# Performance work log

Measured on AMD Instinct MI355X. Metric: run time of the kernel, lower is better.

## Reference

```python
import jax, jax.numpy as jnp
import numpy as np

B, T, F, U, H = 256, 512, 128, 256, 64


def setup_inputs() -> dict:
    key = jax.random.key(0)
    k0, k1, k2, k3, k4 = jax.random.split(key, 5)
    x = jax.random.normal(k0, (B, T, F), dtype=jnp.float32)
    # Keras RandomUniform default range (-0.05, 0.05) for LSTM kernel/bias
    kernel = jax.random.uniform(k1, (F, 4 * U), minval=-0.05, maxval=0.05, dtype=jnp.float32)
    rec_kernel = jax.random.uniform(k2, (U, 4 * U), minval=-0.05, maxval=0.05, dtype=jnp.float32)
    bias = jax.random.uniform(k3, (4 * U,), minval=-0.05, maxval=0.05, dtype=jnp.float32)
    # Dense head: glorot-ish scale for the big [T*U, H] weight
    w_out = jax.random.normal(k4, (T * U, H), dtype=jnp.float32) * (1.0 / np.sqrt(T * U))
    b_out = jnp.zeros((H,), dtype=jnp.float32)
    return {"x": x, "kernel": kernel, "rec_kernel": rec_kernel, "bias": bias,
            "w_out": w_out, "b_out": b_out}


def _lstm_swish(x, kernel, rec_kernel, bias):
    """Keras LSTM with activation=swish, recurrent_activation=sigmoid.
    Gate order along last axis: i, f, c(g), o. Returns full hidden sequence [B,T,U]."""
    b, t, _ = x.shape
    u = rec_kernel.shape[0]
    # Precompute input projections for all timesteps: [B,T,4U]
    xz = jnp.einsum('btf,fg->btg', x, kernel) + bias

    def step(carry, xz_t):
        h, c = carry
        z = xz_t + h @ rec_kernel  # [B,4U]
        zi, zf, zg, zo = jnp.split(z, 4, axis=-1)
        i = jax.nn.sigmoid(zi)
        f = jax.nn.sigmoid(zf)
        g = jax.nn.swish(zg)
        o = jax.nn.sigmoid(zo)
        c_new = f * c + i * g
        h_new = o * jax.nn.swish(c_new)
        return (h_new, c_new), h_new

    h0 = jnp.zeros((b, u), dtype=x.dtype)
    c0 = jnp.zeros((b, u), dtype=x.dtype)
    (_, _), hs = jax.lax.scan(step, (h0, c0), jnp.swapaxes(xz, 0, 1))  # hs: [T,B,U]
    return jnp.swapaxes(hs, 0, 1)  # [B,T,U]


def reference(x, kernel, rec_kernel, bias, w_out, b_out):
    seq = _lstm_swish(x, kernel, rec_kernel, bias)        # [B,T,U]
    flat = seq.reshape(seq.shape[0], -1)                   # [B,T*U]
    return flat @ w_out + b_out                            # [B,horizon]
```

## Files before the change

kernel.cpp:

```cpp
#include <hip/hip_runtime.h>
#include <stdint.h>

#define B_ 256
#define T_ 512
#define F_ 128
#define U_ 256
#define H_ 64
#define G4U (4 * U_)

typedef __attribute__((ext_vector_type(8))) short short8;
typedef __attribute__((ext_vector_type(4))) float f32x4;
typedef unsigned long long ull;

__device__ __forceinline__ uint16_t f2bf(float f) {
  uint32_t u = __builtin_bit_cast(uint32_t, f);
  u += 0x7fffu + ((u >> 16) & 1u);
  return (uint16_t)(u >> 16);
}
__device__ __forceinline__ float sigm(float z) {
  return 1.0f / (1.0f + __expf(-z));
}

__global__ __launch_bounds__(256, 1) void lstm_kernel(
    const float* __restrict__ x, const float* __restrict__ kern,
    const float* __restrict__ rker, const float* __restrict__ bias,
    uint16_t* __restrict__ seq, uint16_t* __restrict__ hbuf,
    uint32_t* __restrict__ ctr)
{
  const int tid  = threadIdx.x;
  const int lane = tid & 63;
  const int wv   = tid >> 6;
  const int bg   = blockIdx.x & 15;
  const int ug   = blockIdx.x >> 4;

  __shared__ __align__(16) uint16_t x_stage[4][64][8];
  __shared__ __align__(16) uint16_t h_stage[8][64][8];
  __shared__ __align__(16) float    z_stage[128][20];

  short8 wf[2][8];
  short8 kf[2][4];
  float  bias_r[2];
  #pragma unroll
  for (int i2 = 0; i2 < 2; ++i2) {
    const int ct   = wv * 2 + i2;
    const int cloc = ct * 16 + (lane & 15);
    const int gcol = (cloc >> 5) * U_ + ug * 32 + (cloc & 31);
    bias_r[i2] = bias[gcol];
    #pragma unroll
    for (int kt = 0; kt < 8; ++kt) {
      short8 v;
      #pragma unroll
      for (int j = 0; j < 8; ++j) {
        const int k = kt * 32 + (lane >> 4) * 8 + j;
        v[j] = (short)f2bf(rker[(size_t)k * G4U + gcol]);
      }
      wf[i2][kt] = v;
    }
    #pragma unroll
    for (int kt = 0; kt < 4; ++kt) {
      short8 v;
      #pragma unroll
      for (int j = 0; j < 8; ++j) {
        const int k = kt * 32 + (lane >> 4) * 8 + j;
        v[j] = (short)f2bf(kern[(size_t)k * G4U + gcol]);
      }
      kf[i2][kt] = v;
    }
  }

  const int xrow = tid & 15;
  const int xfb  = (tid >> 6) * 32 + ((tid >> 4) & 3) * 8;
  const int hrow0 = (tid * 2) & 15;
  const int hub0  = (tid >> 5) * 32 + ((tid >> 3) & 3) * 8;
  const int gr  = tid & 15;
  const int u0  = (tid >> 4) * 2;

  float cst0 = 0.f, cst1 = 0.f;

  float xp[8];
  {
    const float* p = x + ((size_t)(bg * 16 + xrow) * T_ + 0) * F_ + xfb;
    #pragma unroll
    for (int j = 0; j < 8; ++j) xp[j] = p[j];
    uint16_t* d = (uint16_t*)x_stage + tid * 8;
    #pragma unroll
    for (int j = 0; j < 8; ++j) d[j] = f2bf(xp[j]);
  }
  __syncthreads();

  for (int t = 0; t < T_; ++t) {
    f32x4 acc0 = {bias_r[0], bias_r[0], bias_r[0], bias_r[0]};
    f32x4 acc1 = {bias_r[1], bias_r[1], bias_r[1], bias_r[1]};
    #pragma unroll
    for (int kt = 0; kt < 4; ++kt) {
      short8 a = *(const short8*)&x_stage[kt][lane][0];
      acc0 = __builtin_amdgcn_mfma_f32_16x16x32_bf16(a, kf[0][kt], acc0, 0, 0, 0);
      acc1 = __builtin_amdgcn_mfma_f32_16x16x32_bf16(a, kf[1][kt], acc1, 0, 0, 0);
    }
    {
      const int tn = (t + 1 < T_) ? t + 1 : t;
      const float* p = x + ((size_t)(bg * 16 + xrow) * T_ + tn) * F_ + xfb;
      #pragma unroll
      for (int j = 0; j < 8; ++j) xp[j] = p[j];
    }
    {
      const uint32_t target = 8u * (uint32_t)t;
      while (__hip_atomic_load(&ctr[bg], __ATOMIC_RELAXED, __HIP_MEMORY_SCOPE_AGENT) < target)
        __builtin_amdgcn_s_sleep(2);
      __builtin_amdgcn_sched_barrier(0);
    }
    {
      const int cur = t & 1;
      const ull* p = (const ull*)(hbuf + (size_t)cur * (B_ * U_)
                                  + (size_t)(bg * 16 + hrow0) * U_ + hub0);
      ull a0 = __hip_atomic_load(p,      __ATOMIC_RELAXED, __HIP_MEMORY_SCOPE_AGENT);
      ull a1 = __hip_atomic_load(p + 1,  __ATOMIC_RELAXED, __HIP_MEMORY_SCOPE_AGENT);
      ull a2 = __hip_atomic_load(p + 64, __ATOMIC_RELAXED, __HIP_MEMORY_SCOPE_AGENT);
      ull a3 = __hip_atomic_load(p + 65, __ATOMIC_RELAXED, __HIP_MEMORY_SCOPE_AGENT);
      ull* d = (ull*)h_stage + (size_t)tid * 4;
      d[0] = a0; d[1] = a1; d[2] = a2; d[3] = a3;
    }
    __syncthreads();
    #pragma unroll
    for (int kt = 0; kt < 8; ++kt) {
      short8 a = *(const short8*)&h_stage[kt][lane][0];
      acc0 = __builtin_amdgcn_mfma_f32_16x16x32_bf16(a, wf[0][kt], acc0, 0, 0, 0);
      acc1 = __builtin_amdgcn_mfma_f32_16x16x32_bf16(a, wf[1][kt], acc1, 0, 0, 0);
    }
    {
      const int c0 = (wv * 2 + 0) * 16 + (lane & 15);
      const int c1 = (wv * 2 + 1) * 16 + (lane & 15);
      const int r0 = (lane >> 4) * 4;
      *(f32x4*)&z_stage[c0][r0] = acc0;
      *(f32x4*)&z_stage[c1][r0] = acc1;
    }
    __syncthreads();
    {
      const float zi0 = z_stage[u0][gr],      zi1 = z_stage[u0 + 1][gr];
      const float zf0 = z_stage[32 + u0][gr], zf1 = z_stage[33 + u0][gr];
      const float zg0 = z_stage[64 + u0][gr], zg1 = z_stage[65 + u0][gr];
      const float zo0 = z_stage[96 + u0][gr], zo1 = z_stage[97 + u0][gr];
      const float i0 = sigm(zi0), i1 = sigm(zi1);
      const float f0 = sigm(zf0), f1 = sigm(zf1);
      const float g0 = zg0 * sigm(zg0), g1 = zg1 * sigm(zg1);
      const float o0 = sigm(zo0), o1 = sigm(zo1);
      cst0 = f0 * cst0 + i0 * g0;
      cst1 = f1 * cst1 + i1 * g1;
      const float h0 = o0 * (cst0 * sigm(cst0));
      const float h1 = o1 * (cst1 * sigm(cst1));
      const uint32_t packed = (uint32_t)f2bf(h0) | ((uint32_t)f2bf(h1) << 16);
      const int nxt = (t + 1) & 1;
      uint32_t* hd = (uint32_t*)(hbuf + (size_t)nxt * (B_ * U_)
                                 + (size_t)(bg * 16 + gr) * U_ + ug * 32 + u0);
      __hip_atomic_store(hd, packed, __ATOMIC_RELAXED, __HIP_MEMORY_SCOPE_AGENT);
      *(uint32_t*)(seq + ((size_t)(bg * 16 + gr) * T_ + t) * U_ + ug * 32 + u0) = packed;
      uint16_t* d = (uint16_t*)x_stage + tid * 8;
      #pragma unroll
      for (int j = 0; j < 8; ++j) d[j] = f2bf(xp[j]);
    }
    __syncthreads();
    if (tid == 0)
      (void)__hip_atomic_fetch_add(&ctr[bg], 1u, __ATOMIC_RELAXED, __HIP_MEMORY_SCOPE_AGENT);
  }
}

__global__ __launch_bounds__(256, 1) void head_kernel(
    const uint16_t* __restrict__ seq, const float* __restrict__ w_out,
    float* __restrict__ partials)
{
  const int g    = blockIdx.x;
  const int tid  = threadIdx.x;
  const int lane = tid & 63;
  const int wv   = tid >> 6;

  f32x4 acc[4][4];
  #pragma unroll
  for (int i = 0; i < 4; ++i)
    #pragma unroll
    for (int c = 0; c < 4; ++c) acc[i][c] = (f32x4){0.f, 0.f, 0.f, 0.f};

  for (int ks = 0; ks < 64; ++ks) {
    const int krow = g * 2048 + ks * 32 + (lane >> 4) * 8;
    short8 bf[4];
    #pragma unroll
    for (int c = 0; c < 4; ++c) {
      short8 v;
      #pragma unroll
      for (int j = 0; j < 8; ++j)
        v[j] = (short)f2bf(w_out[(size_t)(krow + j) * H_ + c * 16 + (lane & 15)]);
      bf[c] = v;
    }
    #pragma unroll
    for (int i = 0; i < 4; ++i) {
      const int b = (wv * 4 + i) * 16 + (lane & 15);
      short8 a = *(const short8*)(seq + (size_t)b * (T_ * U_) + krow);
      #pragma unroll
      for (int c = 0; c < 4; ++c)
        acc[i][c] = __builtin_amdgcn_mfma_f32_16x16x32_bf16(a, bf[c], acc[i][c], 0, 0, 0);
    }
  }
  #pragma unroll
  for (int i = 0; i < 4; ++i)
    #pragma unroll
    for (int c = 0; c < 4; ++c)
      #pragma unroll
      for (int r = 0; r < 4; ++r) {
        const int b = wv * 64 + i * 16 + (lane >> 4) * 4 + r;
        partials[((size_t)g * B_ + b) * H_ + c * 16 + (lane & 15)] = acc[i][c][r];
      }
}

__global__ void reduce_kernel(const float* __restrict__ partials,
                              const float* __restrict__ b_out,
                              float* __restrict__ out)
{
  const int i = blockIdx.x * 256 + threadIdx.x;
  float s = b_out[i & (H_ - 1)];
  #pragma unroll 8
  for (int g = 0; g < 64; ++g) s += partials[(size_t)g * (B_ * H_) + i];
  out[i] = s;
}

extern "C" void kernel_launch(void* const* d_in, const int* in_sizes, int n_in,
                              void* d_out, int out_size, void* d_ws, size_t ws_size,
                              hipStream_t stream) {
  (void)in_sizes; (void)n_in; (void)out_size; (void)ws_size;
  const float* x     = (const float*)d_in[0];
  const float* kern  = (const float*)d_in[1];
  const float* rker  = (const float*)d_in[2];
  const float* bias  = (const float*)d_in[3];
  const float* w_out = (const float*)d_in[4];
  const float* b_out = (const float*)d_in[5];
  float* out = (float*)d_out;

  char* ws = (char*)d_ws;
  const size_t seq_bytes  = (size_t)B_ * T_ * U_ * 2;
  const size_t hbuf_bytes = (size_t)2 * B_ * U_ * 2;
  uint16_t* seq      = (uint16_t*)ws;
  uint16_t* hbuf     = (uint16_t*)(ws + seq_bytes);
  uint32_t* ctr      = (uint32_t*)(ws + seq_bytes + hbuf_bytes);
  float*    partials = (float*)(ws + seq_bytes + hbuf_bytes + 256);

  hipMemsetAsync(hbuf, 0, (size_t)B_ * U_ * 2, stream);
  hipMemsetAsync(ctr, 0, 64, stream);

  lstm_kernel<<<128, 256, 0, stream>>>(x, kern, rker, bias, seq, hbuf, ctr);
  head_kernel<<<64, 256, 0, stream>>>(seq, w_out, partials);
  reduce_kernel<<<64, 256, 0, stream>>>(partials, b_out, out);
}
```

Before: 1.447 ms.

## Replace counter-based inter-block sync with sequence-tagged hidden-state words

Every hidden-state value is now written as a 64-bit word whose upper half holds the timestep tag. Consumers spin directly on the data until all tags match, so the per-group atomic counter, its increment and the trailing block barrier go away. The x staging write moves before the gate barrier, the first step skips the recurrent matmul, and __syncthreads is replaced by a raw waitcnt plus s_barrier. This removes one barrier and one global atomic round trip from the serial critical path. In exchange it doubles the bytes of h traffic and relies on the atomic 64-bit stores and loads being seen whole.

```diff
diff --git a/kernel.cpp b/kernel.cpp
--- a/kernel.cpp
+++ b/kernel.cpp
@@ -10,7 +10,10 @@
 
 typedef __attribute__((ext_vector_type(8))) short short8;
 typedef __attribute__((ext_vector_type(4))) float f32x4;
+typedef __attribute__((ext_vector_type(4))) uint32_t u32x4;
 typedef unsigned long long ull;
+
+#define BARRIER_LDS() asm volatile("s_waitcnt lgkmcnt(0)\ns_barrier" ::: "memory")
 
 __device__ __forceinline__ uint16_t f2bf(float f) {
   uint32_t u = __builtin_bit_cast(uint32_t, f);
@@ -20,12 +23,14 @@
 __device__ __forceinline__ float sigm(float z) {
   return 1.0f / (1.0f + __expf(-z));
 }
+__device__ __forceinline__ ull ald(const ull* p) {
+  return __hip_atomic_load(p, __ATOMIC_RELAXED, __HIP_MEMORY_SCOPE_AGENT);
+}
 
 __global__ __launch_bounds__(256, 1) void lstm_kernel(
     const float* __restrict__ x, const float* __restrict__ kern,
     const float* __restrict__ rker, const float* __restrict__ bias,
-    uint16_t* __restrict__ seq, uint16_t* __restrict__ hbuf,
-    uint32_t* __restrict__ ctr)
+    uint16_t* __restrict__ seq, ull* __restrict__ hbuf)
 {
   const int tid  = threadIdx.x;
   const int lane = tid & 63;
@@ -70,10 +75,10 @@
 
   const int xrow = tid & 15;
   const int xfb  = (tid >> 6) * 32 + ((tid >> 4) & 3) * 8;
-  const int hrow0 = (tid * 2) & 15;
-  const int hub0  = (tid >> 5) * 32 + ((tid >> 3) & 3) * 8;
   const int gr  = tid & 15;
   const int u0  = (tid >> 4) * 2;
+  const int erow = lane & 15;
+  const int ec0  = (tid >> 6) * 16 + ((lane >> 4) & 3) * 4;
 
   float cst0 = 0.f, cst1 = 0.f;
 
@@ -103,29 +108,34 @@
       #pragma unroll
       for (int j = 0; j < 8; ++j) xp[j] = p[j];
     }
-    {
-      const uint32_t target = 8u * (uint32_t)t;
-      while (__hip_atomic_load(&ctr[bg], __ATOMIC_RELAXED, __HIP_MEMORY_SCOPE_AGENT) < target)
-        __builtin_amdgcn_s_sleep(2);
-      __builtin_amdgcn_sched_barrier(0);
-    }
-    {
-      const int cur = t & 1;
-      const ull* p = (const ull*)(hbuf + (size_t)cur * (B_ * U_)
-                                  + (size_t)(bg * 16 + hrow0) * U_ + hub0);
-      ull a0 = __hip_atomic_load(p,      __ATOMIC_RELAXED, __HIP_MEMORY_SCOPE_AGENT);
-      ull a1 = __hip_atomic_load(p + 1,  __ATOMIC_RELAXED, __HIP_MEMORY_SCOPE_AGENT);
-      ull a2 = __hip_atomic_load(p + 64, __ATOMIC_RELAXED, __HIP_MEMORY_SCOPE_AGENT);
-      ull a3 = __hip_atomic_load(p + 65, __ATOMIC_RELAXED, __HIP_MEMORY_SCOPE_AGENT);
-      ull* d = (ull*)h_stage + (size_t)tid * 4;
-      d[0] = a0; d[1] = a1; d[2] = a2; d[3] = a3;
-    }
-    __syncthreads();
-    #pragma unroll
-    for (int kt = 0; kt < 8; ++kt) {
-      short8 a = *(const short8*)&h_stage[kt][lane][0];
-      acc0 = __builtin_amdgcn_mfma_f32_16x16x32_bf16(a, wf[0][kt], acc0, 0, 0, 0);
-      acc1 = __builtin_amdgcn_mfma_f32_16x16x32_bf16(a, wf[1][kt], acc1, 0, 0, 0);
+    if (t > 0) {
+      const uint32_t expt = (uint32_t)t;
+      const ull* sb = hbuf + (size_t)((t - 1) & 1) * (B_ * 128)
+                           + (size_t)(bg * 16 + erow) * 128;
+      const ull* pa = sb + ec0;
+      const ull* pb = sb + ec0 + 64;
+      ull v0, v1, v2, v3, w0, w1, w2, w3;
+      for (;;) {
+        v0 = ald(pa + 0); v1 = ald(pa + 1); v2 = ald(pa + 2); v3 = ald(pa + 3);
+        w0 = ald(pb + 0); w1 = ald(pb + 1); w2 = ald(pb + 2); w3 = ald(pb + 3);
+        uint32_t bad = ((uint32_t)(v0 >> 32) ^ expt) | ((uint32_t)(v1 >> 32) ^ expt)
+                     | ((uint32_t)(v2 >> 32) ^ expt) | ((uint32_t)(v3 >> 32) ^ expt)
+                     | ((uint32_t)(w0 >> 32) ^ expt) | ((uint32_t)(w1 >> 32) ^ expt)
+                     | ((uint32_t)(w2 >> 32) ^ expt) | ((uint32_t)(w3 >> 32) ^ expt);
+        if (bad == 0u) break;
+      }
+      u32x4* hs = (u32x4*)h_stage;
+      hs[tid]       = (u32x4){(uint32_t)v0, (uint32_t)v1, (uint32_t)v2, (uint32_t)v3};
+      hs[tid + 256] = (u32x4){(uint32_t)w0, (uint32_t)w1, (uint32_t)w2, (uint32_t)w3};
+    }
+    BARRIER_LDS();
+    if (t > 0) {
+      #pragma unroll
+      for (int kt = 0; kt < 8; ++kt) {
+        short8 a = *(const short8*)&h_stage[kt][lane][0];
+        acc0 = __builtin_amdgcn_mfma_f32_16x16x32_bf16(a, wf[0][kt], acc0, 0, 0, 0);
+        acc1 = __builtin_amdgcn_mfma_f32_16x16x32_bf16(a, wf[1][kt], acc1, 0, 0, 0);
+      }
     }
     {
       const int c0 = (wv * 2 + 0) * 16 + (lane & 15);
@@ -133,8 +143,11 @@
       const int r0 = (lane >> 4) * 4;
       *(f32x4*)&z_stage[c0][r0] = acc0;
       *(f32x4*)&z_stage[c1][r0] = acc1;
-    }
-    __syncthreads();
+      uint16_t* d = (uint16_t*)x_stage + tid * 8;
+      #pragma unroll
+      for (int j = 0; j < 8; ++j) d[j] = f2bf(xp[j]);
+    }
+    BARRIER_LDS();
     {
       const float zi0 = z_stage[u0][gr],      zi1 = z_stage[u0 + 1][gr];
       const float zf0 = z_stage[32 + u0][gr], zf1 = z_stage[33 + u0][gr];
@@ -149,18 +162,12 @@
       const float h0 = o0 * (cst0 * sigm(cst0));
       const float h1 = o1 * (cst1 * sigm(cst1));
       const uint32_t packed = (uint32_t)f2bf(h0) | ((uint32_t)f2bf(h1) << 16);
-      const int nxt = (t + 1) & 1;
-      uint32_t* hd = (uint32_t*)(hbuf + (size_t)nxt * (B_ * U_)
-                                 + (size_t)(bg * 16 + gr) * U_ + ug * 32 + u0);
-      __hip_atomic_store(hd, packed, __ATOMIC_RELAXED, __HIP_MEMORY_SCOPE_AGENT);
+      ull* wp = hbuf + (size_t)(t & 1) * (B_ * 128)
+                     + (size_t)(bg * 16 + gr) * 128 + ((ug * 32 + u0) >> 1);
+      __hip_atomic_store(wp, (ull)packed | ((ull)(uint32_t)(t + 1) << 32),
+                         __ATOMIC_RELAXED, __HIP_MEMORY_SCOPE_AGENT);
       *(uint32_t*)(seq + ((size_t)(bg * 16 + gr) * T_ + t) * U_ + ug * 32 + u0) = packed;
-      uint16_t* d = (uint16_t*)x_stage + tid * 8;
-      #pragma unroll
-      for (int j = 0; j < 8; ++j) d[j] = f2bf(xp[j]);
-    }
-    __syncthreads();
-    if (tid == 0)
-      (void)__hip_atomic_fetch_add(&ctr[bg], 1u, __ATOMIC_RELAXED, __HIP_MEMORY_SCOPE_AGENT);
+    }
   }
 }
 
@@ -235,16 +242,14 @@
 
   char* ws = (char*)d_ws;
   const size_t seq_bytes  = (size_t)B_ * T_ * U_ * 2;
-  const size_t hbuf_bytes = (size_t)2 * B_ * U_ * 2;
+  const size_t hbuf_bytes = (size_t)2 * B_ * 128 * 8;
   uint16_t* seq      = (uint16_t*)ws;
-  uint16_t* hbuf     = (uint16_t*)(ws + seq_bytes);
-  uint32_t* ctr      = (uint32_t*)(ws + seq_bytes + hbuf_bytes);
-  float*    partials = (float*)(ws + seq_bytes + hbuf_bytes + 256);
-
-  hipMemsetAsync(hbuf, 0, (size_t)B_ * U_ * 2, stream);
-  hipMemsetAsync(ctr, 0, 64, stream);
-
-  lstm_kernel<<<128, 256, 0, stream>>>(x, kern, rker, bias, seq, hbuf, ctr);
+  ull*      hbuf     = (ull*)(ws + seq_bytes);
+  float*    partials = (float*)(ws + seq_bytes + hbuf_bytes);
+
+  hipMemsetAsync(hbuf, 0, hbuf_bytes, stream);
+
+  lstm_kernel<<<128, 256, 0, stream>>>(x, kern, rker, bias, seq, hbuf);
   head_kernel<<<64, 256, 0, stream>>>(seq, w_out, partials);
   reduce_kernel<<<64, 256, 0, stream>>>(partials, b_out, out);
 }
```

After: 1.477 ms. 2.1% more time.
